# Kernel tuning notes

Hardware: AMD Instinct MI355X
Metric: run time of the kernel (lower is better)

The kernel has to match this reference:

```python
import jax, jax.numpy as jnp
import numpy as np

D_MODEL = 2048
NUM_EXPERTS = 128
TOP_K = 8
NORM_P = 2.0  # normalize_expert_weights


def setup_inputs() -> dict:
    key = jax.random.key(0)
    k1, k2 = jax.random.split(key)
    x = jax.random.normal(k1, (4, 4096, D_MODEL), dtype=jnp.float32)
    # router weight ~ trunc_normal(std=0.02); plain normal*0.02 is fine for a numeric baseline
    weight = jax.random.normal(k2, (NUM_EXPERTS, D_MODEL), dtype=jnp.float32) * 0.02
    score_bias = jnp.zeros((NUM_EXPERTS,), dtype=jnp.float32)
    return {"x": x, "weight": weight, "score_bias": score_bias}


def reference(x, weight, score_bias):
    # Flatten tokens: (B, S, D) -> (N, D); router always runs in fp32 (x.float())
    B, S, D = x.shape
    xf = x.reshape(B * S, D).astype(jnp.float32)
    # get_expert_logits: F.linear(x, weight.view(E, D)) -> (N, E)
    logits = jnp.einsum("nd,ed->ne", xf, weight.astype(jnp.float32))
    # softmax gating
    scores = jax.nn.softmax(logits, axis=-1)
    # bias-adjusted top-k (bias only affects selection, not the returned weights)
    biased = scores + score_bias[None, :]
    _, expert_indices = jax.lax.top_k(biased, TOP_K)          # (N, top_k)
    expert_weights = jnp.take_along_axis(scores, expert_indices, axis=-1)
    # normalize_expert_weights = 2.0 -> divide by L2 norm across top_k
    norm = jnp.linalg.norm(expert_weights, ord=NORM_P, axis=-1, keepdims=True)
    expert_weights = expert_weights / norm
    return expert_weights, expert_indices
```

## Files before the change

kernel.cpp:

```cpp
#include <hip/hip_runtime.h>
#include <hip/hip_bf16.h>
#include <math.h>


#define NE     128
#define TOKT   128
#define KC     32
#define KS     4
#define DMODEL 2048
#define DSLICE (DMODEL / KS)

typedef __attribute__((ext_vector_type(8))) short short8;
typedef __attribute__((ext_vector_type(4))) float f32x4;

union S8 { short s[8]; short8 v; };

__device__ __forceinline__ void split3(float f, S8& hi, S8& mi, S8& lo, int j) {
  const unsigned u0 = __float_as_uint(f);
  const float hif = __uint_as_float(u0 & 0xFFFF0000u);
  const float r1 = f - hif;
  const unsigned u1 = __float_as_uint(r1);
  const float mif = __uint_as_float(u1 & 0xFFFF0000u);
  const float r2 = r1 - mif;
  hi.s[j] = (short)(u0 >> 16);
  mi.s[j] = (short)(u1 >> 16);
  lo.s[j] = (short)(__float_as_uint(r2) >> 16);
}

__global__ __launch_bounds__(256) void logits_mfma(
    const float* __restrict__ x, const float* __restrict__ w,
    float* __restrict__ part, int N) {
  __shared__ short xs[3][TOKT][KC];
  __shared__ short wsm[3][NE][KC];

  const int tid  = threadIdx.x;
  const int wave = tid >> 6;
  const int lane = tid & 63;
  const int wm = wave >> 1;
  const int wn = wave & 1;
  const int quad = lane >> 4;
  const int l16  = lane & 15;
  const size_t tokBase = (size_t)blockIdx.x * TOKT;
  const int d0 = blockIdx.y * DSLICE;

  const int r = tid >> 1;
  const int h = tid & 1;

  f32x4 acc[4][4];
#pragma unroll
  for (int i = 0; i < 4; ++i)
#pragma unroll
    for (int j = 0; j < 4; ++j) acc[i][j] = (f32x4)(0.f);

  for (int kc = 0; kc < DSLICE; kc += KC) {
    __syncthreads();
    {
      const float* gx = x + (tokBase + r) * DMODEL + d0 + kc + h * 16;
      const float* gw = w + (size_t)r * DMODEL + d0 + kc + h * 16;
#pragma unroll
      for (int run = 0; run < 2; ++run) {
        const float4 a0 = *(const float4*)(gx + run * 8);
        const float4 a1 = *(const float4*)(gx + run * 8 + 4);
        S8 hi, mi, lo;
        split3(a0.x, hi, mi, lo, 0); split3(a0.y, hi, mi, lo, 1);
        split3(a0.z, hi, mi, lo, 2); split3(a0.w, hi, mi, lo, 3);
        split3(a1.x, hi, mi, lo, 4); split3(a1.y, hi, mi, lo, 5);
        split3(a1.z, hi, mi, lo, 6); split3(a1.w, hi, mi, lo, 7);
        const int kk = h * 16 + run * 8;
        *(short8*)&xs[0][r][kk] = hi.v;
        *(short8*)&xs[1][r][kk] = mi.v;
        *(short8*)&xs[2][r][kk] = lo.v;
        const float4 b0 = *(const float4*)(gw + run * 8);
        const float4 b1 = *(const float4*)(gw + run * 8 + 4);
        split3(b0.x, hi, mi, lo, 0); split3(b0.y, hi, mi, lo, 1);
        split3(b0.z, hi, mi, lo, 2); split3(b0.w, hi, mi, lo, 3);
        split3(b1.x, hi, mi, lo, 4); split3(b1.y, hi, mi, lo, 5);
        split3(b1.z, hi, mi, lo, 6); split3(b1.w, hi, mi, lo, 7);
        *(short8*)&wsm[0][r][kk] = hi.v;
        *(short8*)&wsm[1][r][kk] = mi.v;
        *(short8*)&wsm[2][r][kk] = lo.v;
      }
    }
    __syncthreads();

    short8 af[4][3];
#pragma unroll
    for (int mt = 0; mt < 4; ++mt)
#pragma unroll
      for (int p = 0; p < 3; ++p)
        af[mt][p] = *(const short8*)&xs[p][wm * 64 + mt * 16 + l16][quad * 8];

#pragma unroll
    for (int nt = 0; nt < 4; ++nt) {
      short8 bf[3];
#pragma unroll
      for (int p = 0; p < 3; ++p)
        bf[p] = *(const short8*)&wsm[p][wn * 64 + nt * 16 + l16][quad * 8];
#pragma unroll
      for (int mt = 0; mt < 4; ++mt) {
        f32x4 c = acc[mt][nt];
        c = __builtin_amdgcn_mfma_f32_16x16x32_bf16(af[mt][0], bf[0], c, 0, 0, 0);
        c = __builtin_amdgcn_mfma_f32_16x16x32_bf16(af[mt][0], bf[1], c, 0, 0, 0);
        c = __builtin_amdgcn_mfma_f32_16x16x32_bf16(af[mt][1], bf[0], c, 0, 0, 0);
        c = __builtin_amdgcn_mfma_f32_16x16x32_bf16(af[mt][0], bf[2], c, 0, 0, 0);
        c = __builtin_amdgcn_mfma_f32_16x16x32_bf16(af[mt][2], bf[0], c, 0, 0, 0);
        c = __builtin_amdgcn_mfma_f32_16x16x32_bf16(af[mt][1], bf[1], c, 0, 0, 0);
        acc[mt][nt] = c;
      }
    }
  }

#pragma unroll
  for (int mt = 0; mt < 4; ++mt)
#pragma unroll
    for (int nt = 0; nt < 4; ++nt) {
      const int ex = wn * 64 + nt * 16 + l16;
#pragma unroll
      for (int reg = 0; reg < 4; ++reg) {
        const size_t tok = tokBase + wm * 64 + mt * 16 + quad * 4 + reg;
        part[((size_t)blockIdx.y * N + tok) * NE + ex] = acc[mt][nt][reg];
      }
    }
}

__global__ __launch_bounds__(256) void router_topk(
    const float* __restrict__ part, const float* __restrict__ bias,
    float* __restrict__ outW, float* __restrict__ outI, int ks, int N) {
  const int wave = threadIdx.x >> 6;
  const int lane = threadIdx.x & 63;
  const int token = blockIdx.x * 4 + wave;
  if (token >= N) return;

  float l0 = 0.f, l1 = 0.f;
  for (int k = 0; k < ks; ++k) {
    const float* p = part + ((size_t)k * N + token) * NE;
    l0 += p[lane];
    l1 += p[lane + 64];
  }

  float m = fmaxf(l0, l1);
#pragma unroll
  for (int off = 1; off < 64; off <<= 1) m = fmaxf(m, __shfl_xor(m, off));
  const float ev0 = __expf(l0 - m);
  const float ev1 = __expf(l1 - m);
  float zs = ev0 + ev1;
#pragma unroll
  for (int off = 1; off < 64; off <<= 1) zs += __shfl_xor(zs, off);
  const float s0 = ev0 / zs;
  const float s1 = ev1 / zs;

  float b0 = s0 + bias[lane];
  float b1 = s1 + bias[lane + 64];

  float myv = 0.f;
  int myi = 0;
  float ss = 0.f;
#pragma unroll
  for (int rnd = 0; rnd < 8; ++rnd) {
    float key; int idx;
    if (b0 >= b1) { key = b0; idx = lane; }
    else          { key = b1; idx = lane + 64; }
#pragma unroll
    for (int off = 1; off < 64; off <<= 1) {
      const float k2 = __shfl_xor(key, off);
      const int   i2 = __shfl_xor(idx, off);
      if (k2 > key || (k2 == key && i2 < idx)) { key = k2; idx = i2; }
    }
    const float cand = (idx < 64) ? s0 : s1;
    const float sw = __shfl(cand, idx & 63);
    ss = fmaf(sw, sw, ss);
    if (lane == rnd) { myv = sw; myi = idx; }
    if (lane == (idx & 63)) { if (idx < 64) b0 = -INFINITY; else b1 = -INFINITY; }
  }

  const float inv = 1.f / sqrtf(ss);
  if (lane < 8) {
    outW[(size_t)token * 8 + lane] = myv * inv;
    outI[(size_t)token * 8 + lane] = (float)myi;
  }
}

extern "C" void kernel_launch(void* const* d_in, const int* in_sizes, int n_in,
                              void* d_out, int out_size, void* d_ws, size_t ws_size,
                              hipStream_t stream) {
  const float* x    = (const float*)d_in[0];
  const float* w    = (const float*)d_in[1];
  const float* bias = (const float*)d_in[2];
  float* out = (float*)d_out;

  const int N = in_sizes[0] / DMODEL;
  float* part = (float*)d_ws;

  logits_mfma<<<dim3(N / TOKT, KS), 256, 0, stream>>>(x, w, part, N);
  router_topk<<<(N + 3) / 4, 256, 0, stream>>>(part, bias, out, out + (size_t)N * 8, KS, N);
}
```

Measured before the change: 223.2 us.

## Fuse router GEMM with softmax top-k and pre-split weights into bf16 chunks

A prep kernel splits the router weights once per call into hi/mid/lo bf16 planes laid out by K-chunk. The main kernel loads those planes straight into LDS with global_load_lds, double-buffers the x and w tiles, and computes full-K logits for 64-token tiles across 8 waves. It then runs softmax and top-k from LDS in the same kernel. This removes the split-K partial-sum buffer and the separate top-k launch, and stops the weights being re-split in every block, but it uses more LDS and registers per block and has less grid parallelism along K.

```diff
diff --git a/kernel.cpp b/kernel.cpp
--- a/kernel.cpp
+++ b/kernel.cpp
@@ -1,21 +1,21 @@
 #include <hip/hip_runtime.h>
-#include <hip/hip_bf16.h>
 #include <math.h>
 
 
-#define NE     128
-#define TOKT   128
-#define KC     32
-#define KS     4
-#define DMODEL 2048
-#define DSLICE (DMODEL / KS)
+#define NE      128
+#define TOKT    64
+#define KC      32
+#define DMODEL  2048
+#define NT      (DMODEL / KC)
+#define CHUNK_SH (3 * NE * KC)
 
 typedef __attribute__((ext_vector_type(8))) short short8;
+typedef __attribute__((ext_vector_type(4))) short s16x4;
 typedef __attribute__((ext_vector_type(4))) float f32x4;
 
-union S8 { short s[8]; short8 v; };
-
-__device__ __forceinline__ void split3(float f, S8& hi, S8& mi, S8& lo, int j) {
+union S4u { short s[4]; s16x4 v; };
+
+__device__ __forceinline__ void split3(float f, S4u& hi, S4u& mi, S4u& lo, int j) {
   const unsigned u0 = __float_as_uint(f);
   const float hif = __uint_as_float(u0 & 0xFFFF0000u);
   const float r1 = f - hif;
@@ -27,77 +27,89 @@
   lo.s[j] = (short)(__float_as_uint(r2) >> 16);
 }
 
-__global__ __launch_bounds__(256) void logits_mfma(
-    const float* __restrict__ x, const float* __restrict__ w,
-    float* __restrict__ part, int N) {
-  __shared__ short xs[3][TOKT][KC];
-  __shared__ short wsm[3][NE][KC];
+__global__ __launch_bounds__(256) void wprep(const float* __restrict__ w,
+                                             short* __restrict__ wp) {
+  const int gid = blockIdx.x * 256 + threadIdx.x;
+  const int e = gid >> 9;
+  const int g = gid & 511;
+  const int k = g << 2;
+  const int chunk = k >> 5;
+  const int kk = k & 31;
+  const f32x4 a = *(const f32x4*)(w + (size_t)e * DMODEL + k);
+  S4u hi, mi, lo;
+  split3(a[0], hi, mi, lo, 0); split3(a[1], hi, mi, lo, 1);
+  split3(a[2], hi, mi, lo, 2); split3(a[3], hi, mi, lo, 3);
+  short* base = wp + (size_t)chunk * CHUNK_SH + (size_t)e * KC + kk;
+  *(s16x4*)(base)               = hi.v;
+  *(s16x4*)(base + NE * KC)     = mi.v;
+  *(s16x4*)(base + 2 * NE * KC) = lo.v;
+}
+
+__device__ __forceinline__ void gll16(const short* g, short* l) {
+  __builtin_amdgcn_global_load_lds(
+      (const __attribute__((address_space(1))) void*)g,
+      (__attribute__((address_space(3))) void*)l, 16, 0, 0);
+}
+
+__global__ __launch_bounds__(512) void router_fused(
+    const float* __restrict__ x, const short* __restrict__ wp,
+    const float* __restrict__ bias, float* __restrict__ outW,
+    float* __restrict__ outI, int N) {
+  __shared__ __align__(16) short xsm[2][3][TOKT][KC];
+  __shared__ __align__(16) short wsm[2][3][NE][KC];
+  __shared__ float L[TOKT][NE + 2];
 
   const int tid  = threadIdx.x;
-  const int wave = tid >> 6;
+  const int wv   = tid >> 6;
   const int lane = tid & 63;
-  const int wm = wave >> 1;
-  const int wn = wave & 1;
+  const int wm   = wv >> 2;
+  const int wn   = wv & 3;
   const int quad = lane >> 4;
   const int l16  = lane & 15;
   const size_t tokBase = (size_t)blockIdx.x * TOKT;
-  const int d0 = blockIdx.y * DSLICE;
-
-  const int r = tid >> 1;
-  const int h = tid & 1;
-
-  f32x4 acc[4][4];
-#pragma unroll
-  for (int i = 0; i < 4; ++i)
-#pragma unroll
-    for (int j = 0; j < 4; ++j) acc[i][j] = (f32x4)(0.f);
-
-  for (int kc = 0; kc < DSLICE; kc += KC) {
-    __syncthreads();
-    {
-      const float* gx = x + (tokBase + r) * DMODEL + d0 + kc + h * 16;
-      const float* gw = w + (size_t)r * DMODEL + d0 + kc + h * 16;
-#pragma unroll
-      for (int run = 0; run < 2; ++run) {
-        const float4 a0 = *(const float4*)(gx + run * 8);
-        const float4 a1 = *(const float4*)(gx + run * 8 + 4);
-        S8 hi, mi, lo;
-        split3(a0.x, hi, mi, lo, 0); split3(a0.y, hi, mi, lo, 1);
-        split3(a0.z, hi, mi, lo, 2); split3(a0.w, hi, mi, lo, 3);
-        split3(a1.x, hi, mi, lo, 4); split3(a1.y, hi, mi, lo, 5);
-        split3(a1.z, hi, mi, lo, 6); split3(a1.w, hi, mi, lo, 7);
-        const int kk = h * 16 + run * 8;
-        *(short8*)&xs[0][r][kk] = hi.v;
-        *(short8*)&xs[1][r][kk] = mi.v;
-        *(short8*)&xs[2][r][kk] = lo.v;
-        const float4 b0 = *(const float4*)(gw + run * 8);
-        const float4 b1 = *(const float4*)(gw + run * 8 + 4);
-        split3(b0.x, hi, mi, lo, 0); split3(b0.y, hi, mi, lo, 1);
-        split3(b0.z, hi, mi, lo, 2); split3(b0.w, hi, mi, lo, 3);
-        split3(b1.x, hi, mi, lo, 4); split3(b1.y, hi, mi, lo, 5);
-        split3(b1.z, hi, mi, lo, 6); split3(b1.w, hi, mi, lo, 7);
-        *(short8*)&wsm[0][r][kk] = hi.v;
-        *(short8*)&wsm[1][r][kk] = mi.v;
-        *(short8*)&wsm[2][r][kk] = lo.v;
-      }
-    }
-    __syncthreads();
-
-    short8 af[4][3];
-#pragma unroll
-    for (int mt = 0; mt < 4; ++mt)
+
+  const int r  = tid >> 3;
+  const int kq = tid & 7;
+  const float* xg = x + (tokBase + r) * (size_t)DMODEL + kq * 4;
+
+  f32x4 accs[4][2][2];
+#pragma unroll
+  for (int s = 0; s < 4; ++s)
+#pragma unroll
+    for (int i = 0; i < 2; ++i)
+#pragma unroll
+      for (int j = 0; j < 2; ++j) accs[s][i][j] = (f32x4)(0.f);
+
+  auto stage_w = [&](int buf, int chunk) {
+    const short* gsrc = wp + (size_t)chunk * CHUNK_SH + wv * 512 + lane * 8;
+    short* ldst = &wsm[buf][0][0][0] + wv * 512;
+    gll16(gsrc,        ldst);
+    gll16(gsrc + 4096, ldst + 4096);
+    gll16(gsrc + 8192, ldst + 8192);
+  };
+  auto stage_x = [&](int buf, f32x4 xr) {
+    S4u hi, mi, lo;
+    split3(xr[0], hi, mi, lo, 0); split3(xr[1], hi, mi, lo, 1);
+    split3(xr[2], hi, mi, lo, 2); split3(xr[3], hi, mi, lo, 3);
+    *(s16x4*)&xsm[buf][0][r][kq * 4] = hi.v;
+    *(s16x4*)&xsm[buf][1][r][kq * 4] = mi.v;
+    *(s16x4*)&xsm[buf][2][r][kq * 4] = lo.v;
+  };
+  auto compute = [&](int buf, f32x4 (&acc)[2][2]) {
+    short8 af[2][3];
+#pragma unroll
+    for (int mt = 0; mt < 2; ++mt)
 #pragma unroll
       for (int p = 0; p < 3; ++p)
-        af[mt][p] = *(const short8*)&xs[p][wm * 64 + mt * 16 + l16][quad * 8];
-
-#pragma unroll
-    for (int nt = 0; nt < 4; ++nt) {
+        af[mt][p] = *(const short8*)&xsm[buf][p][wm * 32 + mt * 16 + l16][quad * 8];
+#pragma unroll
+    for (int nt = 0; nt < 2; ++nt) {
       short8 bf[3];
 #pragma unroll
       for (int p = 0; p < 3; ++p)
-        bf[p] = *(const short8*)&wsm[p][wn * 64 + nt * 16 + l16][quad * 8];
-#pragma unroll
-      for (int mt = 0; mt < 4; ++mt) {
+        bf[p] = *(const short8*)&wsm[buf][p][wn * 32 + nt * 16 + l16][quad * 8];
+#pragma unroll
+      for (int mt = 0; mt < 2; ++mt) {
         f32x4 c = acc[mt][nt];
         c = __builtin_amdgcn_mfma_f32_16x16x32_bf16(af[mt][0], bf[0], c, 0, 0, 0);
         c = __builtin_amdgcn_mfma_f32_16x16x32_bf16(af[mt][0], bf[1], c, 0, 0, 0);
@@ -108,75 +120,92 @@
         acc[mt][nt] = c;
       }
     }
+  };
+
+  stage_w(0, 0);
+  f32x4 xra = *(const f32x4*)(xg);
+  f32x4 xrb = *(const f32x4*)(xg + KC);
+  stage_x(0, xra);
+  __syncthreads();
+
+#pragma unroll
+  for (int s = 0; s < 4; ++s) {
+#pragma unroll 1
+    for (int u = 0; u < 16; u += 2) {
+      const int t = s * 16 + u;
+      if (t + 1 < NT) stage_w(1, t + 1);
+      if (t + 2 < NT) xra = *(const f32x4*)(xg + (t + 2) * KC);
+      compute(0, accs[s]);
+      if (t + 1 < NT) { stage_x(1, xrb); __syncthreads(); }
+      if (t + 2 < NT) stage_w(0, t + 2);
+      if (t + 3 < NT) xrb = *(const f32x4*)(xg + (t + 3) * KC);
+      if (t + 1 < NT) compute(1, accs[s]);
+      if (t + 2 < NT) { stage_x(0, xra); __syncthreads(); }
+    }
   }
 
 #pragma unroll
-  for (int mt = 0; mt < 4; ++mt)
-#pragma unroll
-    for (int nt = 0; nt < 4; ++nt) {
-      const int ex = wn * 64 + nt * 16 + l16;
+  for (int mt = 0; mt < 2; ++mt)
+#pragma unroll
+    for (int nt = 0; nt < 2; ++nt)
 #pragma unroll
       for (int reg = 0; reg < 4; ++reg) {
-        const size_t tok = tokBase + wm * 64 + mt * 16 + quad * 4 + reg;
-        part[((size_t)blockIdx.y * N + tok) * NE + ex] = acc[mt][nt][reg];
+        float v = accs[0][mt][nt][reg];
+        v += accs[1][mt][nt][reg];
+        v += accs[2][mt][nt][reg];
+        v += accs[3][mt][nt][reg];
+        L[wm * 32 + mt * 16 + quad * 4 + reg][wn * 32 + nt * 16 + l16] = v;
       }
-    }
-}
-
-__global__ __launch_bounds__(256) void router_topk(
-    const float* __restrict__ part, const float* __restrict__ bias,
-    float* __restrict__ outW, float* __restrict__ outI, int ks, int N) {
-  const int wave = threadIdx.x >> 6;
-  const int lane = threadIdx.x & 63;
-  const int token = blockIdx.x * 4 + wave;
-  if (token >= N) return;
-
-  float l0 = 0.f, l1 = 0.f;
-  for (int k = 0; k < ks; ++k) {
-    const float* p = part + ((size_t)k * N + token) * NE;
-    l0 += p[lane];
-    l1 += p[lane + 64];
-  }
-
-  float m = fmaxf(l0, l1);
-#pragma unroll
-  for (int off = 1; off < 64; off <<= 1) m = fmaxf(m, __shfl_xor(m, off));
-  const float ev0 = __expf(l0 - m);
-  const float ev1 = __expf(l1 - m);
-  float zs = ev0 + ev1;
-#pragma unroll
-  for (int off = 1; off < 64; off <<= 1) zs += __shfl_xor(zs, off);
-  const float s0 = ev0 / zs;
-  const float s1 = ev1 / zs;
-
-  float b0 = s0 + bias[lane];
-  float b1 = s1 + bias[lane + 64];
-
-  float myv = 0.f;
-  int myi = 0;
-  float ss = 0.f;
-#pragma unroll
-  for (int rnd = 0; rnd < 8; ++rnd) {
-    float key; int idx;
-    if (b0 >= b1) { key = b0; idx = lane; }
-    else          { key = b1; idx = lane + 64; }
-#pragma unroll
-    for (int off = 1; off < 64; off <<= 1) {
-      const float k2 = __shfl_xor(key, off);
-      const int   i2 = __shfl_xor(idx, off);
-      if (k2 > key || (k2 == key && i2 < idx)) { key = k2; idx = i2; }
-    }
-    const float cand = (idx < 64) ? s0 : s1;
-    const float sw = __shfl(cand, idx & 63);
-    ss = fmaf(sw, sw, ss);
-    if (lane == rnd) { myv = sw; myi = idx; }
-    if (lane == (idx & 63)) { if (idx < 64) b0 = -INFINITY; else b1 = -INFINITY; }
-  }
-
-  const float inv = 1.f / sqrtf(ss);
-  if (lane < 8) {
-    outW[(size_t)token * 8 + lane] = myv * inv;
-    outI[(size_t)token * 8 + lane] = (float)myi;
+  __syncthreads();
+
+  const float bmy0 = bias[lane];
+  const float bmy1 = bias[lane + 64];
+  for (int i = 0; i < 8; ++i) {
+    const int tk = wv * 8 + i;
+    const float l0 = L[tk][lane];
+    const float l1 = L[tk][lane + 64];
+
+    float m = fmaxf(l0, l1);
+#pragma unroll
+    for (int off = 1; off < 64; off <<= 1) m = fmaxf(m, __shfl_xor(m, off));
+    const float ev0 = __expf(l0 - m);
+    const float ev1 = __expf(l1 - m);
+    float zs = ev0 + ev1;
+#pragma unroll
+    for (int off = 1; off < 64; off <<= 1) zs += __shfl_xor(zs, off);
+    const float s0 = ev0 / zs;
+    const float s1 = ev1 / zs;
+
+    float b0 = s0 + bmy0;
+    float b1 = s1 + bmy1;
+
+    float myv = 0.f;
+    int myi = 0;
+    float ss = 0.f;
+#pragma unroll
+    for (int rnd = 0; rnd < 8; ++rnd) {
+      float key; int idx;
+      if (b0 >= b1) { key = b0; idx = lane; }
+      else          { key = b1; idx = lane + 64; }
+#pragma unroll
+      for (int off = 1; off < 64; off <<= 1) {
+        const float k2 = __shfl_xor(key, off);
+        const int   i2 = __shfl_xor(idx, off);
+        if (k2 > key || (k2 == key && i2 < idx)) { key = k2; idx = i2; }
+      }
+      const float cand = (idx < 64) ? s0 : s1;
+      const float sw = __shfl(cand, idx & 63);
+      ss = fmaf(sw, sw, ss);
+      if (lane == rnd) { myv = sw; myi = idx; }
+      if (lane == (idx & 63)) { if (idx < 64) b0 = -INFINITY; else b1 = -INFINITY; }
+    }
+
+    const float inv = 1.f / sqrtf(ss);
+    if (lane < 8) {
+      const size_t tok = tokBase + tk;
+      outW[tok * 8 + lane] = myv * inv;
+      outI[tok * 8 + lane] = (float)myi;
+    }
   }
 }
 
@@ -189,8 +218,8 @@
   float* out = (float*)d_out;
 
   const int N = in_sizes[0] / DMODEL;
-  float* part = (float*)d_ws;
-
-  logits_mfma<<<dim3(N / TOKT, KS), 256, 0, stream>>>(x, w, part, N);
-  router_topk<<<(N + 3) / 4, 256, 0, stream>>>(part, bias, out, out + (size_t)N * 8, KS, N);
-}
+  short* wp = (short*)d_ws;
+
+  wprep<<<256, 256, 0, stream>>>(w, wp);
+  router_fused<<<N / TOKT, 512, 0, stream>>>(x, wp, bias, out, out + (size_t)N * 8, N);
+}
```

Result: slower. 271.6 us (+21.7%).
